# Performance work log

Hardware: AMD Instinct MI355X
Metric: run time of the kernel (lower is better)

## Reference

```python
import jax, jax.numpy as jnp
import numpy as np

D_MODEL = 1024
N_HEAD = 16
D_QKV = 64
B, L = 2, 2048
LN_EPS = 1e-5


def setup_inputs() -> dict:
    key = jax.random.key(0)
    ks = jax.random.split(key, 5)
    # xavier-normal-ish scale for [H, d_model, d_qkv] params
    std_in = (2.0 / (D_MODEL + D_QKV)) ** 0.5
    return {
        "x": jax.random.normal(ks[0], (B, L, D_MODEL), jnp.float32),
        "w_q": jax.random.normal(ks[1], (N_HEAD, D_MODEL, D_QKV), jnp.float32) * std_in,
        "w_k": jax.random.normal(ks[2], (N_HEAD, D_MODEL, D_QKV), jnp.float32) * std_in,
        "w_v": jax.random.normal(ks[3], (N_HEAD, D_MODEL, D_QKV), jnp.float32) * std_in,
        "w_o": jax.random.normal(ks[4], (N_HEAD, D_QKV, D_MODEL), jnp.float32) * std_in,
        "ln_gamma": jnp.ones((D_MODEL,), jnp.float32),
        "ln_beta": jnp.zeros((D_MODEL,), jnp.float32),
    }


def reference(x, w_q, w_k, w_v, w_o, ln_gamma, ln_beta):
    # q,k,v: [B, H, L, d_qkv]
    q = jnp.einsum('hmq,blm->bhlq', w_q, x)
    k = jnp.einsum('hmq,blm->bhlq', w_k, x)
    v = jnp.einsum('hmq,blm->bhlq', w_v, x)
    # scores: [B, H, L, L]
    s = jnp.einsum('bhiq,bhjq->bhij', q, k) / (D_QKV ** 0.5)
    s = jax.nn.softmax(s, axis=-1)
    # (dropout disabled: eval-mode reference)
    att = jnp.einsum('bhij,bhjq->bhiq', s, v)          # [B, H, L, d_qkv]
    out = jnp.einsum('bhlq,hqm->blm', att, w_o)        # [B, L, d_model]
    y = x + out                                        # residual
    mu = jnp.mean(y, axis=-1, keepdims=True)
    var = jnp.var(y, axis=-1, keepdims=True)
    return (y - mu) * jax.lax.rsqrt(var + LN_EPS) * ln_gamma + ln_beta
```

## Files before the change

kernel.cpp:

```cpp
#include <hip/hip_runtime.h>
#include <hip/hip_bf16.h>
#include <cstdint>

#define B_      2
#define L_      2048
#define DM_     1024
#define H_      16
#define DQ_     64
#define LN_EPS  1e-5f
#define QSCALE  0.1803368801111204f

typedef unsigned short u16;
typedef unsigned int   u32;
typedef __attribute__((ext_vector_type(8)))  short short8;
typedef __attribute__((ext_vector_type(4)))  unsigned short u16x4;
typedef __attribute__((ext_vector_type(4)))  unsigned int   u32x4;
typedef __attribute__((ext_vector_type(4)))  float f32x4;
typedef __attribute__((ext_vector_type(16))) float f32x16;

__device__ __forceinline__ u16 f2b(float f) {
  __hip_bfloat16 h = __float2bfloat16(f);
  return *reinterpret_cast<u16*>(&h);
}
__device__ __forceinline__ u32 pk2(float lo, float hi) {
  return (u32)f2b(lo) | ((u32)f2b(hi) << 16);
}

__device__ __forceinline__ void gl_lds16(const void* g, void* l) {
  auto gp = reinterpret_cast<const __attribute__((address_space(1))) unsigned int*>(
      reinterpret_cast<uintptr_t>(g));
  auto lp = reinterpret_cast<__attribute__((address_space(3))) unsigned int*>(
      reinterpret_cast<uintptr_t>(l));
  __builtin_amdgcn_global_load_lds(gp, lp, 16, 0, 0);
}

__device__ __forceinline__ short8 frag8(const u16* base, int row, int lchunk) {
  return *(const short8*)(base + row * 64 + ((lchunk ^ (row & 7)) << 3));
}

__global__ __launch_bounds__(256) void prep_all(
    const float* __restrict__ x, const float* __restrict__ wq,
    const float* __restrict__ wk, const float* __restrict__ wv,
    const float* __restrict__ wo, u16* __restrict__ xb,
    u16* __restrict__ wt, u16* __restrict__ wot) {
  __shared__ float Ls[64][65];
  const int t = threadIdx.x;
  const int bx = blockIdx.x;
  if (bx < 4096) {
    int i = bx * 256 + t;
    float4 v = ((const float4*)x)[i];
    u16x4 o = { f2b(v.x), f2b(v.y), f2b(v.z), f2b(v.w) };
    *(u16x4*)(xb + (size_t)i * 4) = o;
  } else if (bx < 4096 + 768) {
    int b2 = bx - 4096;
    int mt = b2 & 15, h = (b2 >> 4) & 15, wh = b2 >> 8;
    const float* in = ((wh == 0) ? wq : (wh == 1) ? wk : wv) + (size_t)h * DM_ * DQ_;
    #pragma unroll
    for (int i = 0; i < 16; ++i) {
      int idx = i * 256 + t, r = idx >> 6, c = idx & 63;
      Ls[r][c] = in[(size_t)(mt * 64 + r) * DQ_ + c];
    }
    __syncthreads();
    u16* outb = wt + (size_t)(wh * H_ + h) * DQ_ * DM_;
    #pragma unroll
    for (int i = 0; i < 16; ++i) {
      int idx = i * 256 + t, q = idx >> 6, mm = idx & 63;
      outb[(size_t)q * DM_ + mt * 64 + mm] = f2b(Ls[mm][q]);
    }
  } else {
    int b3 = bx - 4864;
    int mt = b3 & 15, kt = b3 >> 4;
    #pragma unroll
    for (int i = 0; i < 16; ++i) {
      int idx = i * 256 + t, r = idx >> 6, c = idx & 63;
      Ls[r][c] = wo[(size_t)(kt * 64 + r) * DM_ + mt * 64 + c];
    }
    __syncthreads();
    #pragma unroll
    for (int i = 0; i < 16; ++i) {
      int idx = i * 256 + t, mm = idx >> 6, kk = idx & 63;
      wot[(size_t)(mt * 64 + mm) * DM_ + kt * 64 + kk] = f2b(Ls[kk][mm]);
    }
  }
}

__global__ __launch_bounds__(256) void qkv_big(const u16* __restrict__ xb,
    const u16* __restrict__ wt, u16* __restrict__ Q, u16* __restrict__ K,
    u16* __restrict__ Vtg) {
  const int nt = blockIdx.x, mt = blockIdx.y;
  __shared__ __align__(16) u16 SH[128 * 136];
  u16* As_ = SH;
  u16* Bs_ = SH + 8192;
  const int t = threadIdx.x, w = t >> 6, lane = t & 63;
  const int lx = lane & 15, lq = lane >> 4;
  const int row0 = mt * 128, n0 = nt * 128;
  const int r8 = lane >> 3, lc = (lane & 7) ^ r8;
  const int wr = (w >> 1) * 64, wc = (w & 1) * 64;

  const u16* gA = xb + (size_t)(row0 + w * 32 + r8) * DM_ + lc * 8;
  const u16* gB = wt + (size_t)(n0  + w * 32 + r8) * DM_ + lc * 8;
  u16* lA = As_ + (w * 32) * 64;
  u16* lB = Bs_ + (w * 32) * 64;

  f32x4 z = {0.f, 0.f, 0.f, 0.f};
  f32x4 acc[4][4];
  #pragma unroll
  for (int mb = 0; mb < 4; ++mb)
    #pragma unroll
    for (int nb = 0; nb < 4; ++nb) acc[mb][nb] = z;

  for (int k0 = 0; k0 < DM_; k0 += 64) {
    #pragma unroll
    for (int i = 0; i < 4; ++i) {
      gl_lds16(gA + (size_t)i * 8 * DM_ + k0, lA + i * 8 * 64);
      gl_lds16(gB + (size_t)i * 8 * DM_ + k0, lB + i * 8 * 64);
    }
    __syncthreads();
    short8 af[4][2];
    #pragma unroll
    for (int mb = 0; mb < 4; ++mb)
      #pragma unroll
      for (int kh = 0; kh < 2; ++kh)
        af[mb][kh] = frag8(As_, wr + mb * 16 + lx, (kh << 2) | lq);
    #pragma unroll
    for (int nb = 0; nb < 4; ++nb) {
      short8 b0 = frag8(Bs_, wc + nb * 16 + lx, lq);
      short8 b1 = frag8(Bs_, wc + nb * 16 + lx, 4 | lq);
      #pragma unroll
      for (int mb = 0; mb < 4; ++mb) {
        acc[mb][nb] = __builtin_amdgcn_mfma_f32_16x16x32_bf16(af[mb][0], b0, acc[mb][nb], 0, 0, 0);
        acc[mb][nb] = __builtin_amdgcn_mfma_f32_16x16x32_bf16(af[mb][1], b1, acc[mb][nb], 0, 0, 0);
      }
    }
    __syncthreads();
  }

  const int wh = n0 >> 10;
  const float oscale = (wh == 0) ? QSCALE : 1.0f;
  const int bb = row0 >> 11, l0 = row0 & 2047;
  const int hd0 = n0 & 1023;
  u16* Ep = SH;

  if (wh != 2) {
    #pragma unroll
    for (int mb = 0; mb < 4; ++mb)
      #pragma unroll
      for (int nb = 0; nb < 4; ++nb)
        #pragma unroll
        for (int r = 0; r < 4; ++r) {
          int l = wr + mb * 16 + lq * 4 + r;
          Ep[l * 136 + wc + nb * 16 + lx] = f2b(acc[mb][nb][r] * oscale);
        }
    __syncthreads();
    u16* outp = (wh == 0) ? Q : K;
    #pragma unroll
    for (int hs = 0; hs < 2; ++hs) {
      const int hh = (hd0 >> 6) + hs;
      u16* gbase = outp + ((size_t)(bb * H_ + hh) * L_ + l0) * DQ_;
      #pragma unroll
      for (int it = 0; it < 4; ++it) {
        int u = it * 256 + t;
        int l = u >> 3, chunk = u & 7;
        *(uint4*)(gbase + u * 8) = *(const uint4*)&Ep[l * 136 + hs * 64 + chunk * 8];
      }
    }
  } else {
    #pragma unroll
    for (int mb = 0; mb < 4; ++mb)
      #pragma unroll
      for (int nb = 0; nb < 4; ++nb) {
        int l = wr + mb * 16 + lq * 4;
        int lp = (l & ~12) | ((l & 4) << 1) | ((l & 8) >> 1);
        uint2 pv = { pk2(acc[mb][nb][0], acc[mb][nb][1]),
                     pk2(acc[mb][nb][2], acc[mb][nb][3]) };
        *(uint2*)&Ep[(wc + nb * 16 + lx) * 136 + lp] = pv;
      }
    __syncthreads();
    #pragma unroll
    for (int it = 0; it < 8; ++it) {
      int v = it * 256 + t;
      int dloc = v >> 4, chunk = v & 15;
      int hh = (hd0 + dloc) >> 6, dd = (hd0 + dloc) & 63;
      u16* g = Vtg + ((size_t)(bb * H_ + hh) * DQ_ + dd) * L_ + l0 + chunk * 8;
      *(uint4*)g = *(const uint4*)&Ep[dloc * 136 + chunk * 8];
    }
  }
}

__global__ __launch_bounds__(512) void attn_mfma(const u16* __restrict__ Q,
    const u16* __restrict__ K, const u16* __restrict__ Vtg, u16* __restrict__ att) {
  const int ord = blockIdx.x;
  const int r_  = ord & 7, s_ = ord >> 3;
  const int qt  = s_ & 7, ghi = s_ >> 3;
  const int grp = r_ + 8 * ghi;
  const int h   = grp & 15, b = grp >> 4;
  __shared__ __align__(16) u16 Qs_[256 * 64];
  __shared__ __align__(16) u16 Ks_[2][64 * 64];
  __shared__ __align__(16) u16 Vt_[2][64 * 64];
  const int t = threadIdx.x, w = t >> 6, lane = t & 63;
  const int c = lane & 31, lsel = lane >> 5;
  const int r8 = lane >> 3, lc = (lane & 7) ^ r8;
  const size_t bh  = (size_t)(b * H_ + h) * L_ * DQ_;
  const size_t bhv = (size_t)(b * H_ + h) * DQ_ * L_;

  const u16* gQ = Q + bh + (size_t)(qt * 256 + w * 32 + r8) * DQ_ + lc * 8;
  #pragma unroll
  for (int i = 0; i < 4; ++i) gl_lds16(gQ + (size_t)i * 8 * DQ_, Qs_ + (w * 32 + i * 8) * 64);

  const u16* gK = K   + bh  + (size_t)(w * 8 + r8) * DQ_ + lc * 8;
  const u16* gV = Vtg + bhv + (size_t)(w * 8 + r8) * L_  + lc * 8;

  gl_lds16(gK, Ks_[0] + w * 8 * 64);
  gl_lds16(gV, Vt_[0] + w * 8 * 64);
  __syncthreads();
  short8 qb[4];
  #pragma unroll
  for (int km = 0; km < 4; ++km) qb[km] = frag8(Qs_, w * 32 + c, (km << 1) | lsel);

  f32x16 zz = {0.f,0.f,0.f,0.f,0.f,0.f,0.f,0.f,0.f,0.f,0.f,0.f,0.f,0.f,0.f,0.f};
  f32x16 oacc0 = zz, oacc1 = zz, lacc = zz;
  const short one_bf = (short)0x3F80;
  short8 ones = {one_bf, one_bf, one_bf, one_bf, one_bf, one_bf, one_bf, one_bf};

  for (int kt = 0; kt < L_ / 64; ++kt) {
    const int cur = kt & 1;
    __syncthreads();

    if (kt + 1 < L_ / 64) {
      const int nxt = 1 - cur;
      gl_lds16(gK + (size_t)(kt + 1) * 64 * DQ_, Ks_[nxt] + w * 8 * 64);
      gl_lds16(gV + (size_t)(kt + 1) * 64,       Vt_[nxt] + w * 8 * 64);
    }

    u32x4 paw[4];
    #pragma unroll
    for (int kb = 0; kb < 2; ++kb) {
      f32x16 s = zz;
      #pragma unroll
      for (int km = 0; km < 4; ++km) {
        short8 ka = frag8(Ks_[cur], kb * 32 + c, (km << 1) | lsel);
        s = __builtin_amdgcn_mfma_f32_32x32x16_bf16(ka, qb[km], s, 0, 0, 0);
      }
      #pragma unroll
      for (int F = 0; F < 2; ++F) {
        u32x4 pw;
        #pragma unroll
        for (int i = 0; i < 4; ++i) {
          float p0 = __builtin_amdgcn_exp2f(s[8 * F + 2 * i]);
          float p1 = __builtin_amdgcn_exp2f(s[8 * F + 2 * i + 1]);
          pw[i] = __builtin_amdgcn_perm(__float_as_uint(p1), __float_as_uint(p0), 0x07060302u);
        }
        paw[2 * kb + F] = pw;
      }
    }

    #pragma unroll
    for (int km = 0; km < 4; ++km) {
      short8 pa  = *reinterpret_cast<const short8*>(&paw[km]);
      short8 vb0 = frag8(Vt_[cur], c,      (km << 1) | lsel);
      short8 vb1 = frag8(Vt_[cur], 32 + c, (km << 1) | lsel);
      oacc0 = __builtin_amdgcn_mfma_f32_32x32x16_bf16(pa, vb0, oacc0, 0, 0, 0);
      oacc1 = __builtin_amdgcn_mfma_f32_32x32x16_bf16(pa, vb1, oacc1, 0, 0, 0);
      lacc  = __builtin_amdgcn_mfma_f32_32x32x16_bf16(pa, ones, lacc, 0, 0, 0);
    }
  }

  const int qrow_base = qt * 256 + w * 32;
  #pragma unroll
  for (int r = 0; r < 16; ++r) {
    int qr = (r & 3) + 8 * (r >> 2) + 4 * lsel;
    float inv = 1.0f / lacc[r];
    size_t base = (size_t)(b * L_ + qrow_base + qr) * DM_ + h * DQ_;
    att[base + c]      = f2b(oacc0[r] * inv);
    att[base + 32 + c] = f2b(oacc1[r] * inv);
  }
}

__global__ __launch_bounds__(256) void oproj_big(const u16* __restrict__ A,
    const u16* __restrict__ wot, float* __restrict__ out) {
  const int nt = blockIdx.x, mt = blockIdx.y;
  __shared__ __align__(16) u16 As_[128 * 64];
  __shared__ __align__(16) u16 Bs_[64 * 64];
  const int t = threadIdx.x, w = t >> 6, lane = t & 63;
  const int lx = lane & 15, lq = lane >> 4;
  const int row0 = mt * 128, n0 = nt * 64;
  const int r8 = lane >> 3, lc = (lane & 7) ^ r8;

  const u16* gA = A   + (size_t)(row0 + w * 32 + r8) * DM_ + lc * 8;
  const u16* gB = wot + (size_t)(n0  + w * 16 + r8) * DM_ + lc * 8;
  u16* lA = As_ + (w * 32) * 64;
  u16* lB = Bs_ + (w * 16) * 64;

  f32x4 z = {0.f, 0.f, 0.f, 0.f};
  f32x4 acc[2][4];
  #pragma unroll
  for (int mb = 0; mb < 2; ++mb)
    #pragma unroll
    for (int nb = 0; nb < 4; ++nb) acc[mb][nb] = z;

  for (int k0 = 0; k0 < DM_; k0 += 64) {
    #pragma unroll
    for (int i = 0; i < 4; ++i)
      gl_lds16(gA + (size_t)i * 8 * DM_ + k0, lA + i * 8 * 64);
    #pragma unroll
    for (int i = 0; i < 2; ++i)
      gl_lds16(gB + (size_t)i * 8 * DM_ + k0, lB + i * 8 * 64);
    __syncthreads();
    short8 af[2][2];
    #pragma unroll
    for (int mb = 0; mb < 2; ++mb)
      #pragma unroll
      for (int kh = 0; kh < 2; ++kh)
        af[mb][kh] = frag8(As_, w * 32 + mb * 16 + lx, (kh << 2) | lq);
    #pragma unroll
    for (int nb = 0; nb < 4; ++nb) {
      short8 b0 = frag8(Bs_, nb * 16 + lx, lq);
      short8 b1 = frag8(Bs_, nb * 16 + lx, 4 | lq);
      acc[0][nb] = __builtin_amdgcn_mfma_f32_16x16x32_bf16(af[0][0], b0, acc[0][nb], 0, 0, 0);
      acc[0][nb] = __builtin_amdgcn_mfma_f32_16x16x32_bf16(af[0][1], b1, acc[0][nb], 0, 0, 0);
      acc[1][nb] = __builtin_amdgcn_mfma_f32_16x16x32_bf16(af[1][0], b0, acc[1][nb], 0, 0, 0);
      acc[1][nb] = __builtin_amdgcn_mfma_f32_16x16x32_bf16(af[1][1], b1, acc[1][nb], 0, 0, 0);
    }
    __syncthreads();
  }
  #pragma unroll
  for (int mb = 0; mb < 2; ++mb)
    #pragma unroll
    for (int nb = 0; nb < 4; ++nb)
      #pragma unroll
      for (int r = 0; r < 4; ++r) {
        int row = row0 + w * 32 + mb * 16 + lq * 4 + r;
        out[(size_t)row * DM_ + n0 + nb * 16 + lx] = acc[mb][nb][r];
      }
}

__global__ __launch_bounds__(256) void resid_ln(
    const float* __restrict__ x, const float* __restrict__ gamma,
    const float* __restrict__ beta, float* __restrict__ out) {
  const int row = blockIdx.x;
  const int t   = threadIdx.x;
  const float4* xp = (const float4*)(x   + (size_t)row * DM_);
  float4*       yp = (float4*)      (out + (size_t)row * DM_);

  float4 xv = xp[t];
  float4 av = yp[t];
  float y0 = xv.x + av.x, y1 = xv.y + av.y, y2 = xv.z + av.z, y3 = xv.w + av.w;

  float s  = y0 + y1 + y2 + y3;
  float s2 = y0 * y0 + y1 * y1 + y2 * y2 + y3 * y3;
  #pragma unroll
  for (int off = 32; off > 0; off >>= 1) {
    s  += __shfl_xor(s,  off, 64);
    s2 += __shfl_xor(s2, off, 64);
  }
  __shared__ float red[8];
  const int wave = t >> 6, lane = t & 63;
  if (lane == 0) { red[wave] = s; red[4 + wave] = s2; }
  __syncthreads();
  s  = red[0] + red[1] + red[2] + red[3];
  s2 = red[4] + red[5] + red[6] + red[7];

  const float mean = s * (1.f / DM_);
  const float var  = s2 * (1.f / DM_) - mean * mean;
  const float inv  = rsqrtf(var + LN_EPS);

  const float4 g  = ((const float4*)gamma)[t];
  const float4 bt = ((const float4*)beta)[t];
  float4 r;
  r.x = (y0 - mean) * inv * g.x + bt.x;
  r.y = (y1 - mean) * inv * g.y + bt.y;
  r.z = (y2 - mean) * inv * g.z + bt.z;
  r.w = (y3 - mean) * inv * g.w + bt.w;
  yp[t] = r;
}

extern "C" void kernel_launch(void* const* d_in, const int* in_sizes, int n_in,
                              void* d_out, int out_size, void* d_ws, size_t ws_size,
                              hipStream_t stream) {
  const float* x     = (const float*)d_in[0];
  const float* wq    = (const float*)d_in[1];
  const float* wk    = (const float*)d_in[2];
  const float* wv    = (const float*)d_in[3];
  const float* wo    = (const float*)d_in[4];
  const float* gamma = (const float*)d_in[5];
  const float* beta  = (const float*)d_in[6];
  float* out = (float*)d_out;

  char* ws = (char*)d_ws;
  u16* xb  = (u16*)ws;
  u16* Qb  = (u16*)(ws + ((size_t)8  << 20));
  u16* Kb  = (u16*)(ws + ((size_t)16 << 20));
  u16* Vtg = (u16*)(ws + ((size_t)24 << 20));
  u16* wt  = (u16*)(ws + ((size_t)32 << 20));
  u16* wot = (u16*)(ws + ((size_t)38 << 20));
  u16* att = (u16*)(ws + ((size_t)40 << 20));

  prep_all <<<5120, 256, 0, stream>>>(x, wq, wk, wv, wo, xb, wt, wot);
  qkv_big  <<<dim3(24, 32),    256, 0, stream>>>(xb, wt, Qb, Kb, Vtg);
  attn_mfma<<<256, 512, 0, stream>>>(Qb, Kb, Vtg, att);
  oproj_big<<<dim3(16, 32),    256, 0, stream>>>(att, wot, out);
  resid_ln <<<B_ * L_, 256, 0, stream>>>(x, gamma, beta, out);
}
```

Baseline: 178.3 us.

## Load 128-key chunks per barrier in attention and raise priority around MFMA

The attention loop now stages 128 keys of K and V per double-buffered chunk instead of 64 and processes them as two 64-key halves. This halves the number of block-wide barriers and gives the async loads more compute to hide behind. It also wraps the MFMA sections in s_setprio so that waves issuing matrix ops are scheduled ahead of waves doing exp work. In exchange, LDS use for K/V doubles, which may reduce occupancy.

```diff
diff --git a/kernel.cpp b/kernel.cpp
--- a/kernel.cpp
+++ b/kernel.cpp
@@ -195,8 +195,8 @@
   const int grp = r_ + 8 * ghi;
   const int h   = grp & 15, b = grp >> 4;
   __shared__ __align__(16) u16 Qs_[256 * 64];
-  __shared__ __align__(16) u16 Ks_[2][64 * 64];
-  __shared__ __align__(16) u16 Vt_[2][64 * 64];
+  __shared__ __align__(16) u16 Ks_[2][128 * 64];
+  __shared__ __align__(16) u16 Vt_[2][128 * 64];
   const int t = threadIdx.x, w = t >> 6, lane = t & 63;
   const int c = lane & 31, lsel = lane >> 5;
   const int r8 = lane >> 3, lc = (lane & 7) ^ r8;
@@ -207,11 +207,18 @@
   #pragma unroll
   for (int i = 0; i < 4; ++i) gl_lds16(gQ + (size_t)i * 8 * DQ_, Qs_ + (w * 32 + i * 8) * 64);
 
-  const u16* gK = K   + bh  + (size_t)(w * 8 + r8) * DQ_ + lc * 8;
-  const u16* gV = Vtg + bhv + (size_t)(w * 8 + r8) * L_  + lc * 8;
-
-  gl_lds16(gK, Ks_[0] + w * 8 * 64);
-  gl_lds16(gV, Vt_[0] + w * 8 * 64);
+  const u16* gK = K + bh + (size_t)(w * 16 + r8) * DQ_ + lc * 8;
+  u16* lK0 = Ks_[0] + (w * 16) * 64;
+  u16* lK1 = Ks_[1] + (w * 16) * 64;
+  const int vh = w >> 2, vd = (w & 3) * 16;
+  const u16* gV = Vtg + bhv + (size_t)(vd + r8) * L_ + vh * 64 + lc * 8;
+  u16* lV0 = Vt_[0] + (vh * 64 + vd) * 64;
+  u16* lV1 = Vt_[1] + (vh * 64 + vd) * 64;
+
+  gl_lds16(gK,                   lK0);
+  gl_lds16(gK + (size_t)8 * DQ_, lK0 + 8 * 64);
+  gl_lds16(gV,                   lV0);
+  gl_lds16(gV + (size_t)8 * L_,  lV0 + 8 * 64);
   __syncthreads();
   short8 qb[4];
   #pragma unroll
@@ -222,46 +229,61 @@
   const short one_bf = (short)0x3F80;
   short8 ones = {one_bf, one_bf, one_bf, one_bf, one_bf, one_bf, one_bf, one_bf};
 
-  for (int kt = 0; kt < L_ / 64; ++kt) {
-    const int cur = kt & 1;
-    __syncthreads();
-
-    if (kt + 1 < L_ / 64) {
-      const int nxt = 1 - cur;
-      gl_lds16(gK + (size_t)(kt + 1) * 64 * DQ_, Ks_[nxt] + w * 8 * 64);
-      gl_lds16(gV + (size_t)(kt + 1) * 64,       Vt_[nxt] + w * 8 * 64);
-    }
-
-    u32x4 paw[4];
-    #pragma unroll
-    for (int kb = 0; kb < 2; ++kb) {
-      f32x16 s = zz;
+  for (int ck = 0; ck < L_ / 128; ++ck) {
+    const int cur = ck & 1;
+    __syncthreads();
+
+    if (ck + 1 < L_ / 128) {
+      u16* dK = cur ? lK0 : lK1;
+      u16* dV = cur ? lV0 : lV1;
+      const size_t ko = (size_t)(ck + 1) * 128 * DQ_;
+      const size_t vo = (size_t)(ck + 1) * 128;
+      gl_lds16(gK + ko,                   dK);
+      gl_lds16(gK + ko + (size_t)8 * DQ_, dK + 8 * 64);
+      gl_lds16(gV + vo,                   dV);
+      gl_lds16(gV + vo + (size_t)8 * L_,  dV + 8 * 64);
+    }
+
+    #pragma unroll
+    for (int half = 0; half < 2; ++half) {
+      const u16* Kc = Ks_[cur] + half * 64 * 64;
+      const u16* Vc = Vt_[cur] + half * 64 * 64;
+
+      u32x4 paw[4];
+      #pragma unroll
+      for (int kb = 0; kb < 2; ++kb) {
+        f32x16 s = zz;
+        __builtin_amdgcn_s_setprio(1);
+        #pragma unroll
+        for (int km = 0; km < 4; ++km) {
+          short8 ka = frag8(Kc, kb * 32 + c, (km << 1) | lsel);
+          s = __builtin_amdgcn_mfma_f32_32x32x16_bf16(ka, qb[km], s, 0, 0, 0);
+        }
+        __builtin_amdgcn_s_setprio(0);
+        #pragma unroll
+        for (int F = 0; F < 2; ++F) {
+          u32x4 pw;
+          #pragma unroll
+          for (int i = 0; i < 4; ++i) {
+            float p0 = __builtin_amdgcn_exp2f(s[8 * F + 2 * i]);
+            float p1 = __builtin_amdgcn_exp2f(s[8 * F + 2 * i + 1]);
+            pw[i] = __builtin_amdgcn_perm(__float_as_uint(p1), __float_as_uint(p0), 0x07060302u);
+          }
+          paw[2 * kb + F] = pw;
+        }
+      }
+
+      __builtin_amdgcn_s_setprio(1);
       #pragma unroll
       for (int km = 0; km < 4; ++km) {
-        short8 ka = frag8(Ks_[cur], kb * 32 + c, (km << 1) | lsel);
-        s = __builtin_amdgcn_mfma_f32_32x32x16_bf16(ka, qb[km], s, 0, 0, 0);
-      }
-      #pragma unroll
-      for (int F = 0; F < 2; ++F) {
-        u32x4 pw;
-        #pragma unroll
-        for (int i = 0; i < 4; ++i) {
-          float p0 = __builtin_amdgcn_exp2f(s[8 * F + 2 * i]);
-          float p1 = __builtin_amdgcn_exp2f(s[8 * F + 2 * i + 1]);
-          pw[i] = __builtin_amdgcn_perm(__float_as_uint(p1), __float_as_uint(p0), 0x07060302u);
-        }
-        paw[2 * kb + F] = pw;
-      }
-    }
-
-    #pragma unroll
-    for (int km = 0; km < 4; ++km) {
-      short8 pa  = *reinterpret_cast<const short8*>(&paw[km]);
-      short8 vb0 = frag8(Vt_[cur], c,      (km << 1) | lsel);
-      short8 vb1 = frag8(Vt_[cur], 32 + c, (km << 1) | lsel);
-      oacc0 = __builtin_amdgcn_mfma_f32_32x32x16_bf16(pa, vb0, oacc0, 0, 0, 0);
-      oacc1 = __builtin_amdgcn_mfma_f32_32x32x16_bf16(pa, vb1, oacc1, 0, 0, 0);
-      lacc  = __builtin_amdgcn_mfma_f32_32x32x16_bf16(pa, ones, lacc, 0, 0, 0);
+        short8 pa  = *reinterpret_cast<const short8*>(&paw[km]);
+        short8 vb0 = frag8(Vc, c,      (km << 1) | lsel);
+        short8 vb1 = frag8(Vc, 32 + c, (km << 1) | lsel);
+        oacc0 = __builtin_amdgcn_mfma_f32_32x32x16_bf16(pa, vb0, oacc0, 0, 0, 0);
+        oacc1 = __builtin_amdgcn_mfma_f32_32x32x16_bf16(pa, vb1, oacc1, 0, 0, 0);
+        lacc  = __builtin_amdgcn_mfma_f32_32x32x16_bf16(pa, ones, lacc, 0, 0, 0);
+      }
+      __builtin_amdgcn_s_setprio(0);
     }
   }
 
```

Measured after the change: 176.7 us. About the same (-0.9%).
